# Kernel optimization log

Measured on AMD Instinct MI355X. Metric: run time of the kernel, lower is better.

The kernel has to match this reference:

```python
import jax, jax.numpy as jnp
import numpy as np
from functools import partial

NUM_CLUSTERS = 64
KMEANS_ITERS = 10  # fixed Lloyd iterations standing in for sklearn's converged fit


def _assign(points, centers):
    # points: [M, D], centers: [K, D] -> labels [M]
    # squared L2 distance via expansion; the -|x|^2 term is constant per point
    d = jnp.sum(centers * centers, axis=1)[None, :] - 2.0 * (points @ centers.T)
    return jnp.argmin(d, axis=1)


def _kmeans_fit_predict(points, num_clusters, iters):
    # Deterministic init: first K points (fixed-seed sklearn stand-in).
    centers0 = points[:num_clusters]

    def step(centers, _):
        labels = _assign(points, centers)
        sums = jax.ops.segment_sum(points, labels, num_segments=num_clusters)
        counts = jax.ops.segment_sum(jnp.ones((points.shape[0],), points.dtype),
                                     labels, num_segments=num_clusters)
        new_centers = jnp.where(counts[:, None] > 0, sums / jnp.maximum(counts, 1.0)[:, None], centers)
        return new_centers, None

    centers, _ = jax.lax.scan(step, centers0, None, length=iters)
    labels = _assign(points, centers)
    return labels, centers


def setup_inputs() -> dict:
    key = jax.random.key(0)
    k1, k2, k3 = jax.random.split(key, 3)
    B, N, D = 16, 4096, 384
    x = jax.random.normal(k1, (B, N, D), dtype=jnp.float32)
    # nn.Linear(feature_dim, feature_dim): weight [out, in], bias [out]
    scale = 1.0 / np.sqrt(D)
    W = jax.random.uniform(k2, (D, D), dtype=jnp.float32, minval=-scale, maxval=scale)
    b = jax.random.uniform(k3, (D,), dtype=jnp.float32, minval=-scale, maxval=scale)
    return {"x": x, "W": W, "b": b}


def reference(x, W, b):
    B, N, D = x.shape
    x_flat = jax.lax.stop_gradient(x.reshape(-1, D))  # torch does .detach() before kmeans
    labels, centers = _kmeans_fit_predict(x_flat, NUM_CLUSTERS, KMEANS_ITERS)
    clustered = centers[labels].reshape(B, N, D)
    return clustered @ W.T + b
```

## Files before the change

kernel.cpp:

```cpp
#include <hip/hip_runtime.h>

#define P_TOT 65536
#define DIM   384
#define KCL   64
#define ITERS 10
#define BPTS  256
#define NSB   8
#define BK    32
#define NKT   (DIM / BK)
#define LDA   260
#define LDB   68


__global__ __launch_bounds__(384) void init_kernel(const float* __restrict__ x,
                                                   float* __restrict__ centers,
                                                   float* __restrict__ cnorm,
                                                   float* __restrict__ cnt,
                                                   float* __restrict__ sums) {
    __shared__ float red[384];
    const int c = blockIdx.x, t = threadIdx.x;
    float v = x[(size_t)c * DIM + t];
    centers[(size_t)c * DIM + t] = v;
#pragma unroll
    for (int b = 0; b < NSB; ++b) sums[(size_t)b * KCL * DIM + (size_t)c * DIM + t] = 0.f;
    if (t == 0) cnt[c] = 0.f;
    red[t] = v * v;
    __syncthreads();
    if (t < 128) red[t] = red[t] + red[t + 128] + red[t + 256];
    __syncthreads();
    for (int s = 64; s > 0; s >>= 1) {
        if (t < s) red[t] += red[t + s];
        __syncthreads();
    }
    if (t == 0) cnorm[c] = red[0];
}

#define GEMM_ARGMIN_BODY(X, CENTERS, CNORM)                                          \
    const int t   = threadIdx.x;                                                     \
    const int cg  = t & 7;                                                           \
    const int pg  = t >> 3;                                                          \
    const int p0  = blockIdx.x * BPTS;                                               \
    const int sar = t >> 1;                                \
    const int sak = (t & 1) * 16;                     \
    const int sbr = t >> 3;                                 \
    const int sbk = (t & 7) * 4;                     \
    if (t < KCL) scn[t] = (CNORM)[t];                                                \
    float acc[4][8];                                                                 \
    _Pragma("unroll")                                                                \
    for (int i = 0; i < 4; ++i)                                                      \
        _Pragma("unroll")                                                            \
        for (int j = 0; j < 8; ++j) acc[i][j] = 0.f;                                 \
    const float* xrow = (X) + (size_t)(p0 + sar) * DIM;                              \
    const float* crow = (CENTERS) + (size_t)sbr * DIM;                               \
    float4 ra0 = *(const float4*)(xrow + sak);                                       \
    float4 ra1 = *(const float4*)(xrow + sak + 4);                                   \
    float4 ra2 = *(const float4*)(xrow + sak + 8);                                   \
    float4 ra3 = *(const float4*)(xrow + sak + 12);                                  \
    float4 rb  = *(const float4*)(crow + sbk);                                       \
    for (int kt = 0; kt < NKT; ++kt) {                                               \
        const int cur = kt & 1;                                                      \
        At[cur][sak + 0][sar] = ra0.x;  At[cur][sak + 1][sar] = ra0.y;               \
        At[cur][sak + 2][sar] = ra0.z;  At[cur][sak + 3][sar] = ra0.w;               \
        At[cur][sak + 4][sar] = ra1.x;  At[cur][sak + 5][sar] = ra1.y;               \
        At[cur][sak + 6][sar] = ra1.z;  At[cur][sak + 7][sar] = ra1.w;               \
        At[cur][sak + 8][sar] = ra2.x;  At[cur][sak + 9][sar] = ra2.y;               \
        At[cur][sak + 10][sar] = ra2.z; At[cur][sak + 11][sar] = ra2.w;              \
        At[cur][sak + 12][sar] = ra3.x; At[cur][sak + 13][sar] = ra3.y;              \
        At[cur][sak + 14][sar] = ra3.z; At[cur][sak + 15][sar] = ra3.w;              \
        Bt[cur][sbk + 0][sbr] = rb.x;   Bt[cur][sbk + 1][sbr] = rb.y;                \
        Bt[cur][sbk + 2][sbr] = rb.z;   Bt[cur][sbk + 3][sbr] = rb.w;                \
        if (kt + 1 < NKT) {                        \
            const int k0 = (kt + 1) * BK;                                            \
            ra0 = *(const float4*)(xrow + k0 + sak);                                 \
            ra1 = *(const float4*)(xrow + k0 + sak + 4);                             \
            ra2 = *(const float4*)(xrow + k0 + sak + 8);                             \
            ra3 = *(const float4*)(xrow + k0 + sak + 12);                            \
            rb  = *(const float4*)(crow + k0 + sbk);                                 \
        }                                                                            \
        __syncthreads();                                \
        _Pragma("unroll")                                                            \
        for (int kk = 0; kk < BK; ++kk) {                                            \
            float4 a4 = *(const float4*)&At[cur][kk][pg * 4];                        \
            float4 b0 = *(const float4*)&Bt[cur][kk][cg * 8];                        \
            float4 b1 = *(const float4*)&Bt[cur][kk][cg * 8 + 4];                    \
            const float av[4] = {a4.x, a4.y, a4.z, a4.w};                            \
            const float bv[8] = {b0.x, b0.y, b0.z, b0.w, b1.x, b1.y, b1.z, b1.w};    \
            _Pragma("unroll")                                                        \
            for (int i = 0; i < 4; ++i)                                              \
                _Pragma("unroll")                                                    \
                for (int j = 0; j < 8; ++j) acc[i][j] += av[i] * bv[j];              \
        }                                                                            \
    }                                                                                \
    {                                                                                \
        float cn[8];                                                                 \
        _Pragma("unroll")                                                            \
        for (int j = 0; j < 8; ++j) cn[j] = scn[cg * 8 + j];                         \
        _Pragma("unroll")                                                            \
        for (int i = 0; i < 4; ++i) {                                                \
            float bvv = 3.4e38f; int bc = 0;                                         \
            _Pragma("unroll")                                                        \
            for (int j = 0; j < 8; ++j) {                                            \
                float d = cn[j] - 2.0f * acc[i][j];                                  \
                if (d < bvv) { bvv = d; bc = cg * 8 + j; }                           \
            }                                                                        \
            _Pragma("unroll")                                                        \
            for (int m = 1; m < 8; m <<= 1) {         \
                float ov = __shfl_xor(bvv, m, 64);                                   \
                int   oc = __shfl_xor(bc, m, 64);                                    \
                if (ov < bvv || (ov == bvv && oc < bc)) { bvv = ov; bc = oc; }       \
            }                                                                        \
            if (cg == 0) lab[pg * 4 + i] = bc;             \
        }                                                                            \
    }                                                                                \
    __syncthreads();

__global__ __launch_bounds__(512) void fused_kernel(const float* __restrict__ x,
                                                    const float* __restrict__ centers,
                                                    const float* __restrict__ cnorm,
                                                    float* __restrict__ sums,
                                                    float* __restrict__ cnt) {
    __shared__ float At[2][BK][LDA];
    __shared__ float Bt[2][BK][LDB];
    __shared__ float scn[KCL];
    __shared__ int   lab[BPTS];
    __shared__ int   lcnt[KCL];
    __shared__ int   lstart[KCL + 1];
    __shared__ int   lcur[KCL];
    __shared__ int   order[BPTS];

    if (threadIdx.x < KCL) lcnt[threadIdx.x] = 0;

    GEMM_ARGMIN_BODY(x, centers, cnorm)

    int myl = -1;
    if (t < BPTS) {
        myl = lab[t];
        atomicAdd(&lcnt[myl], 1);
    }
    __syncthreads();
    if (t < 64) {
        int v = lcnt[t];
        int s = v;
#pragma unroll
        for (int d = 1; d < 64; d <<= 1) {
            int u = __shfl_up(s, d, 64);
            if (t >= d) s += u;
        }
        lstart[t] = s - v;
        lcur[t] = s - v;
        if (t == 63) lstart[64] = s;
    }
    __syncthreads();
    if (t < BPTS) {
        int pos = atomicAdd(&lcur[myl], 1);
        order[pos] = t;
    }
    __syncthreads();

    if (t < DIM) {
        const float* xb = x + (size_t)p0 * DIM;
        float* sb = sums + (size_t)(blockIdx.x & (NSB - 1)) * KCL * DIM;
        for (int c = 0; c < KCL; ++c) {
            const int s0 = lstart[c], e0 = lstart[c + 1];
            if (s0 == e0) continue;
            float a0 = 0.f, a1 = 0.f, a2 = 0.f, a3 = 0.f;
            int j = s0;
            for (; j + 3 < e0; j += 4) {
                a0 += xb[(size_t)order[j + 0] * DIM + t];
                a1 += xb[(size_t)order[j + 1] * DIM + t];
                a2 += xb[(size_t)order[j + 2] * DIM + t];
                a3 += xb[(size_t)order[j + 3] * DIM + t];
            }
            for (; j < e0; ++j) a0 += xb[(size_t)order[j] * DIM + t];
            atomicAdd(&sb[c * DIM + t], (a0 + a1) + (a2 + a3));
        }
    }
    if (t < KCL && lcnt[t] > 0) atomicAdd(&cnt[t], (float)lcnt[t]);
}

__global__ __launch_bounds__(512) void label_kernel(const float* __restrict__ x,
                                                    const float* __restrict__ centers,
                                                    const float* __restrict__ cnorm,
                                                    int* __restrict__ labs) {
    __shared__ float At[2][BK][LDA];
    __shared__ float Bt[2][BK][LDB];
    __shared__ float scn[KCL];
    __shared__ int   lab[BPTS];

    GEMM_ARGMIN_BODY(x, centers, cnorm)

    if (t < BPTS) labs[p0 + t] = lab[t];
}

__global__ __launch_bounds__(384) void update_kernel(float* __restrict__ sums,
                                                     float* __restrict__ cnt,
                                                     float* __restrict__ centers,
                                                     float* __restrict__ cnorm) {
    __shared__ float red[384];
    const int c = blockIdx.x, t = threadIdx.x;
    float s = 0.f;
#pragma unroll
    for (int b = 0; b < NSB; ++b) {
        const size_t idx = (size_t)b * KCL * DIM + (size_t)c * DIM + t;
        s += sums[idx];
        sums[idx] = 0.f;
    }
    float n = cnt[c];
    float oldv = centers[(size_t)c * DIM + t];
    float nc = (n > 0.f) ? (s / n) : oldv;
    centers[(size_t)c * DIM + t] = nc;
    red[t] = nc * nc;
    __syncthreads();
    if (t == 0) cnt[c] = 0.f;
    if (t < 128) red[t] = red[t] + red[t + 128] + red[t + 256];
    __syncthreads();
    for (int st = 64; st > 0; st >>= 1) {
        if (t < st) red[t] += red[t + st];
        __syncthreads();
    }
    if (t == 0) cnorm[c] = red[0];
}

__global__ __launch_bounds__(384) void cw_kernel(const float* __restrict__ centers,
                                                 const float* __restrict__ W,
                                                 const float* __restrict__ b,
                                                 float* __restrict__ CW) {
    __shared__ float cs[DIM];
    const int c = blockIdx.x, j = threadIdx.x;
    cs[j] = centers[(size_t)c * DIM + j];
    __syncthreads();
    float acc = b[j];
    const float* wr = W + (size_t)j * DIM;
    for (int d4 = 0; d4 < 96; ++d4) {
        float4 v = *(const float4*)(wr + d4 * 4);
        acc += cs[d4 * 4 + 0] * v.x + cs[d4 * 4 + 1] * v.y
             + cs[d4 * 4 + 2] * v.z + cs[d4 * 4 + 3] * v.w;
    }
    CW[(size_t)c * DIM + j] = acc;
}

__global__ __launch_bounds__(256) void gather_kernel(const int* __restrict__ labs,
                                                     const float* __restrict__ CW,
                                                     float* __restrict__ out) {
    __shared__ int lab[32];
    const int t = threadIdx.x;
    const int p0 = blockIdx.x * 32;
    if (t < 32) lab[t] = labs[p0 + t];
    __syncthreads();
    const int pp = t >> 3;
    const int j0 = t & 7;
    const float* src = CW + (size_t)lab[pp] * DIM;
    float* dst = out + (size_t)(p0 + pp) * DIM;
#pragma unroll
    for (int r = 0; r < 12; ++r) {
        const int jg = (r * 8 + j0) * 4;
        *(float4*)(dst + jg) = *(const float4*)(src + jg);
    }
}

extern "C" void kernel_launch(void* const* d_in, const int* in_sizes, int n_in,
                              void* d_out, int out_size, void* d_ws, size_t ws_size,
                              hipStream_t stream) {
    const float* x = (const float*)d_in[0];
    const float* W = (const float*)d_in[1];
    const float* b = (const float*)d_in[2];
    float* out = (float*)d_out;

    float* centers = (float*)d_ws;
    float* cnorm   = centers + KCL * DIM;
    float* cnt     = cnorm + KCL;
    float* CW      = cnt + KCL;
    float* sums    = CW + KCL * DIM;
    int* labs      = (int*)sums;

    init_kernel<<<KCL, 384, 0, stream>>>(x, centers, cnorm, cnt, sums);
    for (int it = 0; it < ITERS; ++it) {
        fused_kernel<<<P_TOT / BPTS, 512, 0, stream>>>(x, centers, cnorm, sums, cnt);
        update_kernel<<<KCL, 384, 0, stream>>>(sums, cnt, centers, cnorm);
    }
    cw_kernel<<<KCL, 384, 0, stream>>>(centers, W, b, CW);
    label_kernel<<<P_TOT / BPTS, 512, 0, stream>>>(x, centers, cnorm, labs);
    gather_kernel<<<P_TOT / 32, 256, 0, stream>>>(labs, CW, out);
}
```

Before: 1.236 ms.

## Halve points per block and simplify sorted per-cluster accumulation loop

Shrinks the GEMM-argmin tile from 256 to 128 points per block with a 4x4 register tile per thread and a 16-lane argmin reduction, adding occupancy hints to the launch bounds. This doubles the block count so more CUs are busy and cuts registers and shared memory per block. The scatter-sum phase now walks the sorted point order once with a running sum, flushing on cluster changes, instead of looping over all 64 clusters. Risks include lower arithmetic intensity per block, more partial-sum atomics, and an unpadded shared-memory stride that may cause bank conflicts.

```diff
diff --git a/kernel.cpp b/kernel.cpp
--- a/kernel.cpp
+++ b/kernel.cpp
@@ -4,11 +4,11 @@
 #define DIM   384
 #define KCL   64
 #define ITERS 10
-#define BPTS  256
+#define BPTS  128
 #define NSB   8
 #define BK    32
 #define NKT   (DIM / BK)
-#define LDA   260
+#define LDA   128
 #define LDB   68
 
 
@@ -36,75 +36,66 @@
 }
 
 #define GEMM_ARGMIN_BODY(X, CENTERS, CNORM)                                          \
-    const int t   = threadIdx.x;                                                     \
-    const int cg  = t & 7;                                                           \
-    const int pg  = t >> 3;                                                          \
-    const int p0  = blockIdx.x * BPTS;                                               \
-    const int sar = t >> 1;                                \
-    const int sak = (t & 1) * 16;                     \
-    const int sbr = t >> 3;                                 \
-    const int sbk = (t & 7) * 4;                     \
+    const int t    = threadIdx.x;                                                    \
+    const int cg   = t & 15;                              \
+    const int pg   = t >> 4;                         \
+    const int p0   = blockIdx.x * BPTS;                                              \
+    const int sar  = t >> 2;                               \
+    const int sak  = (t & 3) * 4;           \
+    const int sbr  = t >> 3;                                \
+    const int sbk  = (t & 7) * 4;                    \
     if (t < KCL) scn[t] = (CNORM)[t];                                                \
-    float acc[4][8];                                                                 \
+    float acc[4][4];                                                                 \
     _Pragma("unroll")                                                                \
     for (int i = 0; i < 4; ++i)                                                      \
         _Pragma("unroll")                                                            \
-        for (int j = 0; j < 8; ++j) acc[i][j] = 0.f;                                 \
+        for (int j = 0; j < 4; ++j) acc[i][j] = 0.f;                                 \
     const float* xrow = (X) + (size_t)(p0 + sar) * DIM;                              \
     const float* crow = (CENTERS) + (size_t)sbr * DIM;                               \
     float4 ra0 = *(const float4*)(xrow + sak);                                       \
-    float4 ra1 = *(const float4*)(xrow + sak + 4);                                   \
-    float4 ra2 = *(const float4*)(xrow + sak + 8);                                   \
-    float4 ra3 = *(const float4*)(xrow + sak + 12);                                  \
+    float4 ra1 = *(const float4*)(xrow + sak + 16);                                  \
     float4 rb  = *(const float4*)(crow + sbk);                                       \
     for (int kt = 0; kt < NKT; ++kt) {                                               \
         const int cur = kt & 1;                                                      \
         At[cur][sak + 0][sar] = ra0.x;  At[cur][sak + 1][sar] = ra0.y;               \
         At[cur][sak + 2][sar] = ra0.z;  At[cur][sak + 3][sar] = ra0.w;               \
-        At[cur][sak + 4][sar] = ra1.x;  At[cur][sak + 5][sar] = ra1.y;               \
-        At[cur][sak + 6][sar] = ra1.z;  At[cur][sak + 7][sar] = ra1.w;               \
-        At[cur][sak + 8][sar] = ra2.x;  At[cur][sak + 9][sar] = ra2.y;               \
-        At[cur][sak + 10][sar] = ra2.z; At[cur][sak + 11][sar] = ra2.w;              \
-        At[cur][sak + 12][sar] = ra3.x; At[cur][sak + 13][sar] = ra3.y;              \
-        At[cur][sak + 14][sar] = ra3.z; At[cur][sak + 15][sar] = ra3.w;              \
+        At[cur][sak + 16][sar] = ra1.x; At[cur][sak + 17][sar] = ra1.y;              \
+        At[cur][sak + 18][sar] = ra1.z; At[cur][sak + 19][sar] = ra1.w;              \
         Bt[cur][sbk + 0][sbr] = rb.x;   Bt[cur][sbk + 1][sbr] = rb.y;                \
         Bt[cur][sbk + 2][sbr] = rb.z;   Bt[cur][sbk + 3][sbr] = rb.w;                \
         if (kt + 1 < NKT) {                        \
             const int k0 = (kt + 1) * BK;                                            \
             ra0 = *(const float4*)(xrow + k0 + sak);                                 \
-            ra1 = *(const float4*)(xrow + k0 + sak + 4);                             \
-            ra2 = *(const float4*)(xrow + k0 + sak + 8);                             \
-            ra3 = *(const float4*)(xrow + k0 + sak + 12);                            \
+            ra1 = *(const float4*)(xrow + k0 + sak + 16);                            \
             rb  = *(const float4*)(crow + k0 + sbk);                                 \
         }                                                                            \
         __syncthreads();                                \
         _Pragma("unroll")                                                            \
         for (int kk = 0; kk < BK; ++kk) {                                            \
             float4 a4 = *(const float4*)&At[cur][kk][pg * 4];                        \
-            float4 b0 = *(const float4*)&Bt[cur][kk][cg * 8];                        \
-            float4 b1 = *(const float4*)&Bt[cur][kk][cg * 8 + 4];                    \
+            float4 b4 = *(const float4*)&Bt[cur][kk][cg * 4];                        \
             const float av[4] = {a4.x, a4.y, a4.z, a4.w};                            \
-            const float bv[8] = {b0.x, b0.y, b0.z, b0.w, b1.x, b1.y, b1.z, b1.w};    \
+            const float bv[4] = {b4.x, b4.y, b4.z, b4.w};                            \
             _Pragma("unroll")                                                        \
             for (int i = 0; i < 4; ++i)                                              \
                 _Pragma("unroll")                                                    \
-                for (int j = 0; j < 8; ++j) acc[i][j] += av[i] * bv[j];              \
+                for (int j = 0; j < 4; ++j) acc[i][j] += av[i] * bv[j];              \
         }                                                                            \
     }                                                                                \
     {                                                                                \
-        float cn[8];                                                                 \
-        _Pragma("unroll")                                                            \
-        for (int j = 0; j < 8; ++j) cn[j] = scn[cg * 8 + j];                         \
+        float cn[4];                                                                 \
+        _Pragma("unroll")                                                            \
+        for (int j = 0; j < 4; ++j) cn[j] = scn[cg * 4 + j];                         \
         _Pragma("unroll")                                                            \
         for (int i = 0; i < 4; ++i) {                                                \
             float bvv = 3.4e38f; int bc = 0;                                         \
             _Pragma("unroll")                                                        \
-            for (int j = 0; j < 8; ++j) {                                            \
+            for (int j = 0; j < 4; ++j) {                                            \
                 float d = cn[j] - 2.0f * acc[i][j];                                  \
-                if (d < bvv) { bvv = d; bc = cg * 8 + j; }                           \
+                if (d < bvv) { bvv = d; bc = cg * 4 + j; }                           \
             }                                                                        \
             _Pragma("unroll")                                                        \
-            for (int m = 1; m < 8; m <<= 1) {         \
+            for (int m = 1; m < 16; m <<= 1) {       \
                 float ov = __shfl_xor(bvv, m, 64);                                   \
                 int   oc = __shfl_xor(bc, m, 64);                                    \
                 if (ov < bvv || (ov == bvv && oc < bc)) { bvv = ov; bc = oc; }       \
@@ -114,11 +105,11 @@
     }                                                                                \
     __syncthreads();
 
-__global__ __launch_bounds__(512) void fused_kernel(const float* __restrict__ x,
-                                                    const float* __restrict__ centers,
-                                                    const float* __restrict__ cnorm,
-                                                    float* __restrict__ sums,
-                                                    float* __restrict__ cnt) {
+__global__ __launch_bounds__(512, 4) void fused_kernel(const float* __restrict__ x,
+                                                       const float* __restrict__ centers,
+                                                       const float* __restrict__ cnorm,
+                                                       float* __restrict__ sums,
+                                                       float* __restrict__ cnt) {
     __shared__ float At[2][BK][LDA];
     __shared__ float Bt[2][BK][LDB];
     __shared__ float scn[KCL];
@@ -160,28 +151,27 @@
     if (t < DIM) {
         const float* xb = x + (size_t)p0 * DIM;
         float* sb = sums + (size_t)(blockIdx.x & (NSB - 1)) * KCL * DIM;
-        for (int c = 0; c < KCL; ++c) {
-            const int s0 = lstart[c], e0 = lstart[c + 1];
-            if (s0 == e0) continue;
-            float a0 = 0.f, a1 = 0.f, a2 = 0.f, a3 = 0.f;
-            int j = s0;
-            for (; j + 3 < e0; j += 4) {
-                a0 += xb[(size_t)order[j + 0] * DIM + t];
-                a1 += xb[(size_t)order[j + 1] * DIM + t];
-                a2 += xb[(size_t)order[j + 2] * DIM + t];
-                a3 += xb[(size_t)order[j + 3] * DIM + t];
+        int   curc = lab[order[0]];
+        float run  = 0.f;
+        for (int j = 0; j < BPTS; ++j) {
+            const int p = order[j];
+            const int c = lab[p];
+            if (c != curc) {
+                atomicAdd(&sb[curc * DIM + t], run);
+                run = 0.f;
+                curc = c;
             }
-            for (; j < e0; ++j) a0 += xb[(size_t)order[j] * DIM + t];
-            atomicAdd(&sb[c * DIM + t], (a0 + a1) + (a2 + a3));
+            run += xb[(size_t)p * DIM + t];
         }
+        atomicAdd(&sb[curc * DIM + t], run);
     }
     if (t < KCL && lcnt[t] > 0) atomicAdd(&cnt[t], (float)lcnt[t]);
 }
 
-__global__ __launch_bounds__(512) void label_kernel(const float* __restrict__ x,
-                                                    const float* __restrict__ centers,
-                                                    const float* __restrict__ cnorm,
-                                                    int* __restrict__ labs) {
+__global__ __launch_bounds__(512, 4) void label_kernel(const float* __restrict__ x,
+                                                       const float* __restrict__ centers,
+                                                       const float* __restrict__ cnorm,
+                                                       int* __restrict__ labs) {
     __shared__ float At[2][BK][LDA];
     __shared__ float Bt[2][BK][LDB];
     __shared__ float scn[KCL];
```

Measured after the change: 1.227 ms. Within noise of the previous version (-0.7%).
